# Kernel optimization log

Measured on AMD Instinct MI355X. Metric: run time of the kernel, lower is better.

## Reference

```python
import jax, jax.numpy as jnp
import numpy as np

N1 = 10000; N2 = 10000; F_IN = 256
E_EDGES = 480000; P_PAIRS = 200000
HID = 128; H = 8; DH = 16; L = 2


def _segment_softmax(logits, seg, n):
    # softmax over edges sharing the same destination node (per head)
    m = jax.ops.segment_max(logits, seg, num_segments=n)
    m = jnp.where(jnp.isfinite(m), m, 0.0)
    e = jnp.exp(logits - m[seg])
    s = jax.ops.segment_sum(e, seg, num_segments=n)
    return e / (s[seg] + 1e-16)


def _attend(q_dst, k_src, v_src, src, dst, arel, mrel, prior, n_dst):
    # q_dst: [Nd,H,D]; k_src/v_src: [Ns,H,D]; arel/mrel: [H,D,D]; prior: [H]
    k = jnp.einsum('nhd,hde->nhe', k_src, arel)[src]   # [E,H,D]
    v = jnp.einsum('nhd,hde->nhe', v_src, mrel)[src]   # [E,H,D]
    logits = jnp.einsum('ehd,ehd->eh', q_dst[dst], k) * prior / jnp.sqrt(jnp.asarray(DH, q_dst.dtype))
    a = _segment_softmax(logits, dst, n_dst)           # [E,H]
    out = jax.ops.segment_sum(a[..., None] * v, dst, num_segments=n_dst)
    return out.reshape(n_dst, HID)


def _forward(x_n1, x_n2, Win1, bin1, Win2, bin2, Wk, bk, Wq, bq, Wv, bv, Wa, ba, skip, arel, mrel, prior, ei12, ei21, edge_index):
    proj = lambda x, W, b: (x @ W + b).reshape(-1, H, DH)
    h1 = jax.nn.relu(x_n1 @ Win1 + bin1)
    h2 = jax.nn.relu(x_n2 @ Win2 + bin2)
    feats1, feats2 = [], []
    for l in range(L):
        k1, q1, v1 = proj(h1, Wk[l, 0], bk[l, 0]), proj(h1, Wq[l, 0], bq[l, 0]), proj(h1, Wv[l, 0], bv[l, 0])
        k2, q2, v2 = proj(h2, Wk[l, 1], bk[l, 1]), proj(h2, Wq[l, 1], bq[l, 1]), proj(h2, Wv[l, 1], bv[l, 1])
        # edge type 0: n1 -> n2 (dst = n2); edge type 1: n2 -> n1 (dst = n1)
        agg2 = _attend(q2, k1, v1, ei12[0], ei12[1], arel[l, 0], mrel[l, 0], prior[l, 0], N2)
        agg1 = _attend(q1, k2, v2, ei21[0], ei21[1], arel[l, 1], mrel[l, 1], prior[l, 1], N1)
        o1 = jax.nn.gelu(agg1) @ Wa[l, 0] + ba[l, 0]
        o2 = jax.nn.gelu(agg2) @ Wa[l, 1] + ba[l, 1]
        s1 = jax.nn.sigmoid(skip[l, 0]); s2 = jax.nn.sigmoid(skip[l, 1])
        h1 = s1 * o1 + (1.0 - s1) * h1
        h2 = s2 * o2 + (1.0 - s2) * h2
        feats1.append(h1); feats2.append(h2)
    Em = jnp.concatenate(feats1, axis=1)   # [N1, HID*L]
    Ed = jnp.concatenate(feats2, axis=1)   # [N2, HID*L]
    # scores = Em @ Ed.T then gather at (m_index, d_index); computed as gathered dot
    # products (same math, avoids [N1,N2] materialization). Dropout in eval mode.
    preds = jnp.einsum('pc,pc->p', Em[edge_index[0]], Ed[edge_index[1]])[:, None]
    return preds


def setup_inputs():
    key = jax.random.key(0)
    ks = jax.random.split(key, 16)
    sc = 0.05
    inp = {}
    inp['x_n1'] = jax.random.normal(ks[0], (N1, F_IN), jnp.float32)
    inp['x_n2'] = jax.random.normal(ks[1], (N2, F_IN), jnp.float32)
    inp['ei12'] = jnp.stack([jax.random.randint(ks[2], (E_EDGES,), 0, N1),
                             jax.random.randint(ks[3], (E_EDGES,), 0, N2)])
    inp['ei21'] = jnp.stack([jax.random.randint(ks[4], (E_EDGES,), 0, N2),
                             jax.random.randint(ks[5], (E_EDGES,), 0, N1)])
    inp['edge_index'] = jnp.stack([jax.random.randint(ks[6], (P_PAIRS,), 0, N1),
                                   jax.random.randint(ks[7], (P_PAIRS,), 0, N2)])
    inp['Win1'] = jax.random.normal(ks[8], (F_IN, HID), jnp.float32) * sc
    inp['bin1'] = jnp.zeros((HID,), jnp.float32)
    inp['Win2'] = jax.random.normal(ks[9], (F_IN, HID), jnp.float32) * sc
    inp['bin2'] = jnp.zeros((HID,), jnp.float32)
    inp['Wk'] = jax.random.normal(ks[10], (L, 2, HID, HID), jnp.float32) * sc
    inp['bk'] = jnp.zeros((L, 2, HID), jnp.float32)
    inp['Wq'] = jax.random.normal(ks[11], (L, 2, HID, HID), jnp.float32) * sc
    inp['bq'] = jnp.zeros((L, 2, HID), jnp.float32)
    inp['Wv'] = jax.random.normal(ks[12], (L, 2, HID, HID), jnp.float32) * sc
    inp['bv'] = jnp.zeros((L, 2, HID), jnp.float32)
    inp['Wa'] = jax.random.normal(ks[13], (L, 2, HID, HID), jnp.float32) * sc
    inp['ba'] = jnp.zeros((L, 2, HID), jnp.float32)
    inp['skip'] = jnp.ones((L, 2), jnp.float32)
    inp['arel'] = jax.random.normal(ks[14], (L, 2, H, DH, DH), jnp.float32) * 0.25
    inp['mrel'] = jax.random.normal(ks[15], (L, 2, H, DH, DH), jnp.float32) * 0.25
    inp['prior'] = jnp.ones((L, 2, H), jnp.float32)
    return inp


def reference(x_n1, x_n2, ei12, ei21, edge_index, Win1, bin1, Win2, bin2, Wk, bk, Wq, bq, Wv, bv, Wa, ba, skip, arel, mrel, prior):
    return _forward(x_n1, x_n2, Win1, bin1, Win2, bin2, Wk, bk, Wq, bq, Wv, bv, Wa, ba, skip, arel, mrel, prior, ei12, ei21, edge_index)
```

## Files before the change

### kernel.cpp

```cpp
#include <hip/hip_runtime.h>
#include <math.h>

#define N1c 10000
#define N2c 10000
#define F_INc 256
#define Ec 480000
#define Pc 200000
#define Lc 2
#define NPART 32
#define NPc 313
#define NBLK 256
#define CAPE 17408
#define CAPP 7936

using short8 = __attribute__((ext_vector_type(8))) short;
using float4v = __attribute__((ext_vector_type(4))) float;
using floatx2 = __attribute__((ext_vector_type(2))) float;

__device__ __forceinline__ float gelu_f(float x) {
    const float k0 = 0.7978845608028654f;
    const float k1 = 0.044715f;
    float x3 = x * x * x;
    float t = tanhf(k0 * (x + k1 * x3));
    return 0.5f * x * (1.0f + t);
}

__device__ __forceinline__ float bf2f(unsigned short x) {
    union { unsigned int u; float f; } c;
    c.u = ((unsigned int)x) << 16;
    return c.f;
}
__device__ __forceinline__ unsigned short f2bf(float f) {
    union { float f; unsigned int u; } c;
    c.f = f;
    unsigned int u = c.u;
    unsigned int r = (u + 0x7FFFu + ((u >> 16) & 1u)) >> 16;
    return (unsigned short)r;
}
__device__ __forceinline__ unsigned char f2fp8(float v) {
    unsigned int p = __builtin_amdgcn_cvt_pk_fp8_f32(v, v, 0u, false);
    return (unsigned char)(p & 0xFF);
}

__global__ __launch_bounds__(256) void prep_kernel(
    const float* __restrict__ Wq, const float* __restrict__ bq,
    const float* __restrict__ Wk, const float* __restrict__ bk,
    const float* __restrict__ Wv, const float* __restrict__ bv,
    const float* __restrict__ arel, const float* __restrict__ mrel,
    const float* __restrict__ prior,
    const float* __restrict__ Win1, const float* __restrict__ Win2,
    const float* __restrict__ Wa,
    short* __restrict__ Wqkvt, float* __restrict__ bqkv,
    short* __restrict__ Wint1, short* __restrict__ Wint2, short* __restrict__ Wat,
    int* __restrict__ gcnt)
{
    if (blockIdx.x == 0 && threadIdx.x < 3 * NPART) gcnt[threadIdx.x] = 0;
    int id = blockIdx.x * 256 + threadIdx.x;
    if (id < 196608) {
        int lt = id / 49152;
        int r = id - lt * 49152;
        int col = r >> 7, c = r & 127;
        short* Wout = Wqkvt + (size_t)lt * 384 * 128;
        float* bout = bqkv + lt * 384;
        if (col < 128) {
            Wout[col * 128 + c] = (short)f2bf(Wq[lt * 16384 + c * 128 + col]);
            if (c == 0) bout[col] = bq[lt * 128 + col];
            return;
        }
        int which = (col < 256) ? 0 : 1;
        int he = col - (which ? 256 : 128);
        int h = he >> 4, e = he & 15;
        const float* W = (which == 0 ? Wk : Wv) + lt * 16384;
        const float* b = (which == 0 ? bk : bv) + lt * 128;
        const float* R = (which == 0 ? arel : mrel) + lt * 2048;
        float sc = (which == 0) ? prior[lt * 8 + h] * 0.25f : 1.0f;
        float acc = 0.f;
        #pragma unroll
        for (int d = 0; d < 16; d++)
            acc += W[c * 128 + h * 16 + d] * R[(h * 16 + d) * 16 + e];
        Wout[col * 128 + c] = (short)f2bf(acc * sc);
        if (c == 0) {
            float bacc = 0.f;
            #pragma unroll
            for (int d = 0; d < 16; d++)
                bacc += b[h * 16 + d] * R[(h * 16 + d) * 16 + e];
            bout[col] = bacc * sc;
        }
    } else {
        int wid = id - 196608;
        if (wid < 65536) {
            int y = wid >> 15;
            int id2 = wid & 32767;
            int n = id2 >> 8, k = id2 & 255;
            const float* W = y ? Win2 : Win1;
            short* O = y ? Wint2 : Wint1;
            O[n * 256 + k] = (short)f2bf(W[k * 128 + n]);
        } else {
            int wid2 = wid - 65536;
            int lt = wid2 >> 14;
            int id2 = wid2 & 16383;
            int n = id2 >> 7, k = id2 & 127;
            Wat[lt * 16384 + n * 128 + k] = (short)f2bf(Wa[lt * 16384 + k * 128 + n]);
        }
    }
}

__global__ __launch_bounds__(256) void scatter_bins_kernel(
    const int* __restrict__ ei12, const int* __restrict__ ei21, const int* __restrict__ eidx,
    int* __restrict__ gcnt,
    unsigned int* __restrict__ stg12, unsigned int* __restrict__ stg21,
    unsigned int* __restrict__ stgm)
{
    int blk = blockIdx.x, z = blockIdx.y, t = threadIdx.x;
    const int* key; const int* pay; int E; unsigned int* stg; int cap;
    if (z == 0)      { key = ei12 + Ec; pay = ei12; E = Ec; stg = stg12; cap = CAPE; }
    else if (z == 1) { key = ei21 + Ec; pay = ei21; E = Ec; stg = stg21; cap = CAPE; }
    else             { key = eidx;      pay = nullptr; E = Pc; stg = stgm; cap = CAPP; }
    int chunk = (E + NBLK - 1) / NBLK;
    int start = blk * chunk;
    int stop = min(start + chunk, E);
    __shared__ int cnt[NPART];
    __shared__ int base[NPART];
    __shared__ int fill[NPART];
    if (t < NPART) cnt[t] = 0;
    __syncthreads();
    for (int e = start + t; e < stop; e += 256)
        atomicAdd(&cnt[key[e] / NPc], 1);
    __syncthreads();
    if (t < NPART) {
        base[t] = cnt[t] ? atomicAdd(&gcnt[z * NPART + t], cnt[t]) : 0;
        fill[t] = 0;
    }
    __syncthreads();
    for (int e = start + t; e < stop; e += 256) {
        unsigned int k = (unsigned int)key[e];
        int p = (int)(k / NPc);
        int r = atomicAdd(&fill[p], 1);
        unsigned int pk = (z == 2) ? ((k << 18) | (unsigned int)e)
                                   : ((k << 14) | (unsigned int)pay[e]);
        stg[(size_t)p * cap + base[p] + r] = pk;
    }
}

__global__ __launch_bounds__(256) void build_csr_kernel(
    const int* __restrict__ gcnt,
    const unsigned int* __restrict__ stg12, const unsigned int* __restrict__ stg21,
    const unsigned int* __restrict__ stgm,
    int* __restrict__ rp12, int* __restrict__ rp21, int* __restrict__ rpm,
    int* __restrict__ es12, int* __restrict__ es21, int* __restrict__ ps)
{
    int p = blockIdx.x, z = blockIdx.y, t = threadIdx.x;
    const unsigned int* stg; int* rowptr; int* out; int cap;
    if (z == 0)      { stg = stg12; rowptr = rp12; out = es12; cap = CAPE; }
    else if (z == 1) { stg = stg21; rowptr = rp21; out = es21; cap = CAPE; }
    else             { stg = stgm;  rowptr = rpm;  out = ps;   cap = CAPP; }
    int ksh = (z == 2) ? 18 : 14;
    unsigned int pmask = (z == 2) ? 0x3FFFFu : 0x3FFFu;
    int baseOut = 0, cntP = 0;
    #pragma unroll
    for (int j = 0; j < NPART; j++) {
        int c = gcnt[z * NPART + j];
        if (j < p) baseOut += c;
        if (j == p) cntP = c;
    }
    const unsigned int* sbase = stg + (size_t)p * cap;
    int lo = p * NPc;
    int hi = min(lo + NPc, 10000);

    __shared__ int hist[512];
    __shared__ int fill[NPc];
    hist[t] = 0; hist[t + 256] = 0;
    __syncthreads();
    for (int i = t; i < cntP; i += 256)
        atomicAdd(&hist[(int)(sbase[i] >> ksh) - lo], 1);
    __syncthreads();
    for (int off = 1; off < 512; off <<= 1) {
        int i0 = t, i1 = t + 256;
        int v0 = (i0 >= off) ? hist[i0 - off] : 0;
        int v1 = (i1 >= off) ? hist[i1 - off] : 0;
        __syncthreads();
        hist[i0] += v0; hist[i1] += v1;
        __syncthreads();
    }
    for (int i = t; i < NPc; i += 256) {
        int excl = i ? hist[i - 1] : 0;
        fill[i] = excl;
        if (lo + i < hi) rowptr[lo + i] = baseOut + excl;
    }
    if (p == NPART - 1 && t == 0) rowptr[10000] = baseOut + cntP;
    __syncthreads();
    for (int i = t; i < cntP; i += 256) {
        unsigned int pk = sbase[i];
        int r = atomicAdd(&fill[(int)(pk >> ksh) - lo], 1);
        out[baseOut + r] = (int)(pk & pmask);
    }
}

template<int A_GELU, int OUT_RELU, int SKIP, int PACKQKV, int ABF, int KT>
__global__ __launch_bounds__(256) void gemm_mfma(
    const void* __restrict__ A0v, const void* __restrict__ A1v, int ldA,
    const short* __restrict__ Wt0, const short* __restrict__ Wt1,
    const float* __restrict__ b0, const float* __restrict__ b1,
    unsigned short* __restrict__ C0, unsigned short* __restrict__ C1, int ldC,
    unsigned char* __restrict__ KV8o0, unsigned char* __restrict__ KV8o1,
    int M,
    const float* __restrict__ sk0, const float* __restrict__ sk1,
    const unsigned short* __restrict__ H0, const unsigned short* __restrict__ H1, int ldH)
{
    int z = blockIdx.z;
    const void* Av = z ? A1v : A0v;
    const short* Wt = z ? Wt1 : Wt0;
    const float* bias = z ? b1 : b0;
    unsigned short* C = z ? C1 : C0;
    unsigned char* KV8o = z ? KV8o1 : KV8o0;
    const float* skipv = z ? sk1 : sk0;
    const unsigned short* Hold = z ? H1 : H0;

    __shared__ short Alds[64 * 40];
    __shared__ short Blds[64 * 40];

    int tid = threadIdx.x;
    int w = tid >> 6;
    int l = tid & 63;
    int mBase = blockIdx.x * 64;
    int nBase = blockIdx.y * 64;

    int srow = tid >> 2;
    int koct = tid & 3;

    float4v acc[4];
    #pragma unroll
    for (int i = 0; i < 4; i++) acc[i] = (float4v){0.f, 0.f, 0.f, 0.f};

    int arow = mBase + srow;
    const short* Wptr = Wt + (size_t)(nBase + srow) * KT + koct * 8;

    int fl = l & 15;
    int fo = (l >> 4) * 8;

    #pragma unroll
    for (int k0 = 0; k0 < KT; k0 += 32) {
        uint4 raw;
        if (ABF) {
            const unsigned short* Ab = (const unsigned short*)Av;
            raw = make_uint4(0u, 0u, 0u, 0u);
            if (arow < M) raw = *(const uint4*)(Ab + (size_t)arow * ldA + k0 + koct * 8);
            if (A_GELU) {
                unsigned int wd[4] = {raw.x, raw.y, raw.z, raw.w};
                #pragma unroll
                for (int i = 0; i < 4; i++) {
                    float lo = gelu_f(bf2f((unsigned short)(wd[i] & 0xFFFFu)));
                    float hi = gelu_f(bf2f((unsigned short)(wd[i] >> 16)));
                    wd[i] = (unsigned int)f2bf(lo) | ((unsigned int)f2bf(hi) << 16);
                }
                raw = make_uint4(wd[0], wd[1], wd[2], wd[3]);
            }
        } else {
            const float* Af = (const float*)Av;
            float av[8];
            if (arow < M) {
                const float4* p = (const float4*)(Af + (size_t)arow * ldA + k0 + koct * 8);
                float4 f0 = p[0], f1 = p[1];
                av[0]=f0.x; av[1]=f0.y; av[2]=f0.z; av[3]=f0.w;
                av[4]=f1.x; av[5]=f1.y; av[6]=f1.z; av[7]=f1.w;
            } else {
                #pragma unroll
                for (int i = 0; i < 8; i++) av[i] = 0.f;
            }
            unsigned int pk[4];
            #pragma unroll
            for (int i = 0; i < 4; i++)
                pk[i] = (unsigned int)f2bf(av[2*i]) | ((unsigned int)f2bf(av[2*i+1]) << 16);
            raw = make_uint4(pk[0], pk[1], pk[2], pk[3]);
        }
        *(uint4*)&Alds[srow * 40 + koct * 8] = raw;
        *(uint4*)&Blds[srow * 40 + koct * 8] = *(const uint4*)(Wptr + k0);
        __syncthreads();

        short8 bfr = *(const short8*)&Blds[(w * 16 + fl) * 40 + fo];
        #pragma unroll
        for (int msub = 0; msub < 4; msub++) {
            short8 afr = *(const short8*)&Alds[(msub * 16 + fl) * 40 + fo];
            acc[msub] = __builtin_amdgcn_mfma_f32_16x16x32_bf16(afr, bfr, acc[msub], 0, 0, 0);
        }
        __syncthreads();
    }

    float sig = 0.f;
    if (SKIP) sig = 1.f / (1.f + __expf(-skipv[0]));
    int col = nBase + w * 16 + fl;
    float bcol = bias[col];
    int rbase = mBase + ((l >> 4) * 4);
    #pragma unroll
    for (int msub = 0; msub < 4; msub++) {
        #pragma unroll
        for (int r = 0; r < 4; r++) {
            int row = rbase + msub * 16 + r;
            if (row >= M) continue;
            float v = acc[msub][r] + bcol;
            if (OUT_RELU) v = fmaxf(v, 0.f);
            if (SKIP) v = sig * v + (1.f - sig) * bf2f(Hold[(size_t)row * ldH + col]);
            if (PACKQKV) {
                if (col < 128) {
                    C[(size_t)row * ldC + col] = f2bf(v);
                } else if (col < 256) {
                    int c = col - 128;
                    KV8o[(size_t)row * 256 + (c >> 3) * 16 + (c & 7)] = f2fp8(v);
                } else {
                    int c = col - 256;
                    KV8o[(size_t)row * 256 + (c >> 3) * 16 + 8 + (c & 7)] = f2fp8(v);
                }
            } else {
                C[(size_t)row * ldC + col] = f2bf(v);
            }
        }
    }
}

__global__ __launch_bounds__(128) void attend_kernel(
    const unsigned short* __restrict__ Qb1, const unsigned char* __restrict__ KV81,
    const unsigned short* __restrict__ Qb2, const unsigned char* __restrict__ KV82,
    const int* __restrict__ rp12, const int* __restrict__ es12,
    const int* __restrict__ rp21, const int* __restrict__ es21,
    unsigned short* __restrict__ agg1, unsigned short* __restrict__ agg2)
{
    int b = blockIdx.x;
    const unsigned short* Qb; const unsigned char* KV; const int* rp; const int* es;
    unsigned short* outb; int n;
    if (b < 1250) { n = b * 8 + (threadIdx.x >> 4);          Qb = Qb2; KV = KV81; rp = rp12; es = es12; outb = agg2; }
    else          { n = (b - 1250) * 8 + (threadIdx.x >> 4); Qb = Qb1; KV = KV82; rp = rp21; es = es21; outb = agg1; }
    int ln = threadIdx.x & 15;

    float q[8];
    {
        const ushort4* qp = (const ushort4*)(Qb + (size_t)n * 128 + 8 * ln);
        ushort4 qa = qp[0], qc = qp[1];
        q[0]=bf2f(qa.x); q[1]=bf2f(qa.y); q[2]=bf2f(qa.z); q[3]=bf2f(qa.w);
        q[4]=bf2f(qc.x); q[5]=bf2f(qc.y); q[6]=bf2f(qc.z); q[7]=bf2f(qc.w);
    }
    int beg = rp[n], end = rp[n + 1];
    float s = 0.f;
    float acc[8];
    #pragma unroll
    for (int c = 0; c < 8; c++) acc[c] = 0.f;

    auto dec8 = [&](unsigned int w0, unsigned int w1, float* d) {
        floatx2 a0 = __builtin_amdgcn_cvt_pk_f32_fp8(w0, false);
        floatx2 a1 = __builtin_amdgcn_cvt_pk_f32_fp8(w0, true);
        floatx2 a2 = __builtin_amdgcn_cvt_pk_f32_fp8(w1, false);
        floatx2 a3 = __builtin_amdgcn_cvt_pk_f32_fp8(w1, true);
        d[0]=a0[0]; d[1]=a0[1]; d[2]=a1[0]; d[3]=a1[1];
        d[4]=a2[0]; d[5]=a2[1]; d[6]=a3[0]; d[7]=a3[1];
    };
    auto proc1 = [&](uint4 kv) {
        float kd[8], vd[8];
        dec8(kv.x, kv.y, kd);
        float p = q[0]*kd[0] + q[1]*kd[1] + q[2]*kd[2] + q[3]*kd[3]
                + q[4]*kd[4] + q[5]*kd[5] + q[6]*kd[6] + q[7]*kd[7];
        p += __shfl_xor(p, 1, 2);
        float x = __expf(p);
        s += x;
        dec8(kv.z, kv.w, vd);
        #pragma unroll
        for (int c = 0; c < 8; c++) acc[c] += x * vd[c];
    };
    auto ld = [&](int e) { return *(const uint4*)(KV + (size_t)e * 256 + 16 * ln); };

    int i = beg;
    int pre = min(end, (beg + 3) & ~3);
    for (; i < pre; i++) proc1(ld(es[i]));
    for (; i + 8 <= end; i += 8) {
        int4 ea = *(const int4*)&es[i];
        int4 eb = *(const int4*)&es[i + 4];
        uint4 w0 = ld(ea.x), w1 = ld(ea.y), w2 = ld(ea.z), w3 = ld(ea.w);
        uint4 w4 = ld(eb.x), w5 = ld(eb.y), w6 = ld(eb.z), w7 = ld(eb.w);
        proc1(w0); proc1(w1); proc1(w2); proc1(w3);
        proc1(w4); proc1(w5); proc1(w6); proc1(w7);
    }
    for (; i + 4 <= end; i += 4) {
        int4 ea = *(const int4*)&es[i];
        uint4 w0 = ld(ea.x), w1 = ld(ea.y), w2 = ld(ea.z), w3 = ld(ea.w);
        proc1(w0); proc1(w1); proc1(w2); proc1(w3);
    }
    for (; i < end; i++) proc1(ld(es[i]));

    float inv = 1.f / (s + 1e-16f);
    unsigned int w0 = (unsigned int)f2bf(acc[0]*inv) | ((unsigned int)f2bf(acc[1]*inv) << 16);
    unsigned int w1 = (unsigned int)f2bf(acc[2]*inv) | ((unsigned int)f2bf(acc[3]*inv) << 16);
    unsigned int w2 = (unsigned int)f2bf(acc[4]*inv) | ((unsigned int)f2bf(acc[5]*inv) << 16);
    unsigned int w3 = (unsigned int)f2bf(acc[6]*inv) | ((unsigned int)f2bf(acc[7]*inv) << 16);
    *(uint4*)(outb + (size_t)n * 128 + 8 * ln) = make_uint4(w0, w1, w2, w3);
}

__global__ __launch_bounds__(256) void pred_kernel(
    const unsigned short* __restrict__ Emb, const unsigned short* __restrict__ Edb,
    const int* __restrict__ eidx,
    const int* __restrict__ rpm, const int* __restrict__ porder,
    float* __restrict__ out)
{
    int m = blockIdx.x * 4 + (threadIdx.x >> 6);
    int l = threadIdx.x & 63;
    int g = l >> 4;
    int ln = l & 15;
    int beg = rpm[m], end = rpm[m + 1];
    if (beg == end) return;
    float a[16];
    {
        const uint4* ap = (const uint4*)(Emb + (size_t)m * 256 + 16 * ln);
        uint4 u0 = ap[0], u1 = ap[1];
        unsigned int wv[8] = {u0.x, u0.y, u0.z, u0.w, u1.x, u1.y, u1.z, u1.w};
        #pragma unroll
        for (int i = 0; i < 8; i++) {
            a[2*i]   = bf2f((unsigned short)(wv[i] & 0xFFFFu));
            a[2*i+1] = bf2f((unsigned short)(wv[i] >> 16));
        }
    }
    for (int i = beg + g; i < end; i += 4) {
        int p = porder[i];
        int d = eidx[Pc + p];
        const uint4* bp = (const uint4*)(Edb + (size_t)d * 256 + 16 * ln);
        uint4 u0 = bp[0], u1 = bp[1];
        unsigned int wv[8] = {u0.x, u0.y, u0.z, u0.w, u1.x, u1.y, u1.z, u1.w};
        float s = 0.f;
        #pragma unroll
        for (int j = 0; j < 8; j++)
            s += a[2*j] * bf2f((unsigned short)(wv[j] & 0xFFFFu))
               + a[2*j+1] * bf2f((unsigned short)(wv[j] >> 16));
        s += __shfl_xor(s, 1, 16);
        s += __shfl_xor(s, 2, 16);
        s += __shfl_xor(s, 4, 16);
        s += __shfl_xor(s, 8, 16);
        if (ln == 0) out[p] = s;
    }
}

extern "C" void kernel_launch(void* const* d_in, const int* in_sizes, int n_in,
                              void* d_out, int out_size, void* d_ws, size_t ws_size,
                              hipStream_t stream)
{
    const float* x1   = (const float*)d_in[0];
    const float* x2   = (const float*)d_in[1];
    const int*   ei12 = (const int*)d_in[2];
    const int*   ei21 = (const int*)d_in[3];
    const int*   eidx = (const int*)d_in[4];
    const float* Win1 = (const float*)d_in[5];
    const float* bin1 = (const float*)d_in[6];
    const float* Win2 = (const float*)d_in[7];
    const float* bin2 = (const float*)d_in[8];
    const float* Wk   = (const float*)d_in[9];
    const float* bk   = (const float*)d_in[10];
    const float* Wq   = (const float*)d_in[11];
    const float* bq   = (const float*)d_in[12];
    const float* Wv   = (const float*)d_in[13];
    const float* bv   = (const float*)d_in[14];
    const float* Wa   = (const float*)d_in[15];
    const float* ba   = (const float*)d_in[16];
    const float* skip = (const float*)d_in[17];
    const float* arel = (const float*)d_in[18];
    const float* mrel = (const float*)d_in[19];
    const float* prior= (const float*)d_in[20];

    char* ws = (char*)d_ws;
    size_t off = 0;
    auto allocB = [&](size_t bytes) { void* p = ws + off; off += (bytes + 15) & ~15ull; return p; };
    auto allocF = [&](size_t n) { return (float*)allocB(n * 4); };
    auto allocI = [&](size_t n) { return (int*)allocB(n * 4); };
    auto allocS = [&](size_t n) { return (short*)allocB(n * 2); };
    auto allocU = [&](size_t n) { return (unsigned short*)allocB(n * 2); };

    unsigned short* h1b  = allocU((size_t)N1c * 128);
    unsigned short* h2b  = allocU((size_t)N2c * 128);
    unsigned short* Qb1  = allocU((size_t)N1c * 128);
    unsigned short* Qb2  = allocU((size_t)N2c * 128);
    unsigned char*  KV81 = (unsigned char*)allocB((size_t)N1c * 256);
    unsigned char*  KV82 = (unsigned char*)allocB((size_t)N2c * 256);
    unsigned short* agg1 = allocU((size_t)N1c * 128);
    unsigned short* agg2 = allocU((size_t)N2c * 128);
    unsigned short* Emb  = allocU((size_t)N1c * 256);
    unsigned short* Edb  = allocU((size_t)N2c * 256);
    float* bqkv  = allocF(4 * 384);
    short* Wqkvt = allocS(4 * 384 * 128);
    short* Wint1 = allocS(128 * 256);
    short* Wint2 = allocS(128 * 256);
    short* Wat   = allocS(4 * 128 * 128);
    int* rp12  = allocI(N2c + 1);
    int* rp21  = allocI(N1c + 1);
    int* rpm   = allocI(N1c + 1);
    int* es12  = allocI(Ec);
    int* es21  = allocI(Ec);
    int* ps    = allocI(Pc);
    int* gcnt  = allocI(3 * NPART);
    unsigned int* stg12 = (unsigned int*)allocB((size_t)NPART * CAPE * 4);
    unsigned int* stg21 = (unsigned int*)allocB((size_t)NPART * CAPE * 4);
    unsigned int* stgm  = (unsigned int*)allocB((size_t)NPART * CAPP * 4);

    prep_kernel<<<1280, 256, 0, stream>>>(
        Wq, bq, Wk, bk, Wv, bv, arel, mrel, prior,
        Win1, Win2, Wa, Wqkvt, bqkv, Wint1, Wint2, Wat, gcnt);

    scatter_bins_kernel<<<dim3(NBLK, 3), 256, 0, stream>>>(
        ei12, ei21, eidx, gcnt, stg12, stg21, stgm);
    build_csr_kernel<<<dim3(NPART, 3), 256, 0, stream>>>(
        gcnt, stg12, stg21, stgm, rp12, rp21, rpm, es12, es21, ps);

    const int MB = (N1c + 63) / 64;
    gemm_mfma<0, 1, 0, 0, 0, 256><<<dim3(MB, 2, 2), 256, 0, stream>>>(
        x1, x2, F_INc, Wint1, Wint2, bin1, bin2, h1b, h2b, 128,
        nullptr, nullptr,
        N1c, nullptr, nullptr, nullptr, nullptr, 0);

    for (int l = 0; l < Lc; l++) {
        const unsigned short* A1 = (l == 0) ? h1b : Emb;  int ld1 = (l == 0) ? 128 : 256;
        const unsigned short* A2 = (l == 0) ? h2b : Edb;
        int lt0 = l * 2 + 0, lt1 = l * 2 + 1;
        gemm_mfma<0, 0, 0, 1, 1, 128><<<dim3(MB, 6, 2), 256, 0, stream>>>(
            A1, A2, ld1,
            Wqkvt + (size_t)lt0 * 49152, Wqkvt + (size_t)lt1 * 49152,
            bqkv + lt0 * 384, bqkv + lt1 * 384,
            Qb1, Qb2, 128,
            KV81, KV82,
            N1c, nullptr, nullptr, nullptr, nullptr, 0);
        attend_kernel<<<(N1c + N2c) / 8, 128, 0, stream>>>(
            Qb1, KV81, Qb2, KV82, rp12, es12, rp21, es21, agg1, agg2);
        gemm_mfma<1, 0, 1, 0, 1, 128><<<dim3(MB, 2, 2), 256, 0, stream>>>(
            agg1, agg2, 128,
            Wat + (size_t)lt0 * 16384, Wat + (size_t)lt1 * 16384,
            ba + lt0 * 128, ba + lt1 * 128,
            Emb + l * 128, Edb + l * 128, 256,
            nullptr, nullptr,
            N1c,
            skip + lt0, skip + lt1,
            A1, A2, ld1);
    }

    pred_kernel<<<N1c / 4, 256, 0, stream>>>(Emb, Edb, eidx, rpm, ps, (float*)d_out);
}
```

Before: 304.4 us.

## Split attention edges across two half-waves and widen QKV GEMM tiles

The attend kernel now assigns 32 lanes per destination node instead of 16, with each 16-lane group processing half of the node's edge list. The partial sums and softmax denominators are then combined with a cross-lane shuffle. This doubles the parallelism available for gather latency, at the cost of twice as many blocks and extra shuffle work. Separately, the QKV GEMM gets an NS template parameter so each block computes two 64-column N-tiles, reusing the A tile from LDS across both and halving the number of blocks that reload A.

```diff
diff --git a/kernel.cpp b/kernel.cpp
--- a/kernel.cpp
+++ b/kernel.cpp
@@ -196,7 +196,7 @@
     }
 }
 
-template<int A_GELU, int OUT_RELU, int SKIP, int PACKQKV, int ABF, int KT>
+template<int A_GELU, int OUT_RELU, int SKIP, int PACKQKV, int ABF, int KT, int NS>
 __global__ __launch_bounds__(256) void gemm_mfma(
     const void* __restrict__ A0v, const void* __restrict__ A1v, int ldA,
     const short* __restrict__ Wt0, const short* __restrict__ Wt1,
@@ -217,23 +217,24 @@
     const unsigned short* Hold = z ? H1 : H0;
 
     __shared__ short Alds[64 * 40];
-    __shared__ short Blds[64 * 40];
+    __shared__ short Blds[64 * NS * 40];
 
     int tid = threadIdx.x;
     int w = tid >> 6;
     int l = tid & 63;
     int mBase = blockIdx.x * 64;
-    int nBase = blockIdx.y * 64;
+    int nBase = blockIdx.y * 64 * NS;
 
     int srow = tid >> 2;
     int koct = tid & 3;
 
-    float4v acc[4];
+    float4v acc[NS][4];
     #pragma unroll
-    for (int i = 0; i < 4; i++) acc[i] = (float4v){0.f, 0.f, 0.f, 0.f};
+    for (int s = 0; s < NS; s++)
+        #pragma unroll
+        for (int i = 0; i < 4; i++) acc[s][i] = (float4v){0.f, 0.f, 0.f, 0.f};
 
     int arow = mBase + srow;
-    const short* Wptr = Wt + (size_t)(nBase + srow) * KT + koct * 8;
 
     int fl = l & 15;
     int fo = (l >> 4) * 8;
@@ -274,44 +275,55 @@
             raw = make_uint4(pk[0], pk[1], pk[2], pk[3]);
         }
         *(uint4*)&Alds[srow * 40 + koct * 8] = raw;
-        *(uint4*)&Blds[srow * 40 + koct * 8] = *(const uint4*)(Wptr + k0);
+        #pragma unroll
+        for (int r = 0; r < NS; r++) {
+            int nrow = nBase + r * 64 + srow;
+            *(uint4*)&Blds[(r * 64 + srow) * 40 + koct * 8] =
+                *(const uint4*)(Wt + (size_t)nrow * KT + k0 + koct * 8);
+        }
         __syncthreads();
 
-        short8 bfr = *(const short8*)&Blds[(w * 16 + fl) * 40 + fo];
-        #pragma unroll
-        for (int msub = 0; msub < 4; msub++) {
-            short8 afr = *(const short8*)&Alds[(msub * 16 + fl) * 40 + fo];
-            acc[msub] = __builtin_amdgcn_mfma_f32_16x16x32_bf16(afr, bfr, acc[msub], 0, 0, 0);
+        #pragma unroll
+        for (int s = 0; s < NS; s++) {
+            short8 bfr = *(const short8*)&Blds[(s * 64 + w * 16 + fl) * 40 + fo];
+            #pragma unroll
+            for (int msub = 0; msub < 4; msub++) {
+                short8 afr = *(const short8*)&Alds[(msub * 16 + fl) * 40 + fo];
+                acc[s][msub] = __builtin_amdgcn_mfma_f32_16x16x32_bf16(afr, bfr, acc[s][msub], 0, 0, 0);
+            }
         }
         __syncthreads();
     }
 
     float sig = 0.f;
     if (SKIP) sig = 1.f / (1.f + __expf(-skipv[0]));
-    int col = nBase + w * 16 + fl;
-    float bcol = bias[col];
     int rbase = mBase + ((l >> 4) * 4);
     #pragma unroll
-    for (int msub = 0; msub < 4; msub++) {
-        #pragma unroll
-        for (int r = 0; r < 4; r++) {
-            int row = rbase + msub * 16 + r;
-            if (row >= M) continue;
-            float v = acc[msub][r] + bcol;
-            if (OUT_RELU) v = fmaxf(v, 0.f);
-            if (SKIP) v = sig * v + (1.f - sig) * bf2f(Hold[(size_t)row * ldH + col]);
-            if (PACKQKV) {
-                if (col < 128) {
+    for (int s = 0; s < NS; s++) {
+        int col = nBase + s * 64 + w * 16 + fl;
+        float bcol = bias[col];
+        #pragma unroll
+        for (int msub = 0; msub < 4; msub++) {
+            #pragma unroll
+            for (int r = 0; r < 4; r++) {
+                int row = rbase + msub * 16 + r;
+                if (row >= M) continue;
+                float v = acc[s][msub][r] + bcol;
+                if (OUT_RELU) v = fmaxf(v, 0.f);
+                if (SKIP) v = sig * v + (1.f - sig) * bf2f(Hold[(size_t)row * ldH + col]);
+                if (PACKQKV) {
+                    if (col < 128) {
+                        C[(size_t)row * ldC + col] = f2bf(v);
+                    } else if (col < 256) {
+                        int c = col - 128;
+                        KV8o[(size_t)row * 256 + (c >> 3) * 16 + (c & 7)] = f2fp8(v);
+                    } else {
+                        int c = col - 256;
+                        KV8o[(size_t)row * 256 + (c >> 3) * 16 + 8 + (c & 7)] = f2fp8(v);
+                    }
+                } else {
                     C[(size_t)row * ldC + col] = f2bf(v);
-                } else if (col < 256) {
-                    int c = col - 128;
-                    KV8o[(size_t)row * 256 + (c >> 3) * 16 + (c & 7)] = f2fp8(v);
-                } else {
-                    int c = col - 256;
-                    KV8o[(size_t)row * 256 + (c >> 3) * 16 + 8 + (c & 7)] = f2fp8(v);
                 }
-            } else {
-                C[(size_t)row * ldC + col] = f2bf(v);
             }
         }
     }
@@ -325,11 +337,14 @@
     unsigned short* __restrict__ agg1, unsigned short* __restrict__ agg2)
 {
     int b = blockIdx.x;
+    int nid = threadIdx.x >> 5;
+    int l32 = threadIdx.x & 31;
+    int g = l32 >> 4;
+    int ln = l32 & 15;
     const unsigned short* Qb; const unsigned char* KV; const int* rp; const int* es;
     unsigned short* outb; int n;
-    if (b < 1250) { n = b * 8 + (threadIdx.x >> 4);          Qb = Qb2; KV = KV81; rp = rp12; es = es12; outb = agg2; }
-    else          { n = (b - 1250) * 8 + (threadIdx.x >> 4); Qb = Qb1; KV = KV82; rp = rp21; es = es21; outb = agg1; }
-    int ln = threadIdx.x & 15;
+    if (b < 2500) { n = b * 4 + nid;          Qb = Qb2; KV = KV81; rp = rp12; es = es12; outb = agg2; }
+    else          { n = (b - 2500) * 4 + nid; Qb = Qb1; KV = KV82; rp = rp21; es = es21; outb = agg1; }
 
     float q[8];
     {
@@ -339,6 +354,11 @@
         q[4]=bf2f(qc.x); q[5]=bf2f(qc.y); q[6]=bf2f(qc.z); q[7]=bf2f(qc.w);
     }
     int beg = rp[n], end = rp[n + 1];
+    int cnt = end - beg;
+    int half = (cnt + 1) >> 1;
+    int gbeg = beg + g * half;
+    int gend = g ? end : (beg + half);
+
     float s = 0.f;
     float acc[8];
     #pragma unroll
@@ -366,10 +386,10 @@
     };
     auto ld = [&](int e) { return *(const uint4*)(KV + (size_t)e * 256 + 16 * ln); };
 
-    int i = beg;
-    int pre = min(end, (beg + 3) & ~3);
+    int i = gbeg;
+    int pre = min(gend, (gbeg + 3) & ~3);
     for (; i < pre; i++) proc1(ld(es[i]));
-    for (; i + 8 <= end; i += 8) {
+    for (; i + 8 <= gend; i += 8) {
         int4 ea = *(const int4*)&es[i];
         int4 eb = *(const int4*)&es[i + 4];
         uint4 w0 = ld(ea.x), w1 = ld(ea.y), w2 = ld(ea.z), w3 = ld(ea.w);
@@ -377,19 +397,25 @@
         proc1(w0); proc1(w1); proc1(w2); proc1(w3);
         proc1(w4); proc1(w5); proc1(w6); proc1(w7);
     }
-    for (; i + 4 <= end; i += 4) {
+    for (; i + 4 <= gend; i += 4) {
         int4 ea = *(const int4*)&es[i];
         uint4 w0 = ld(ea.x), w1 = ld(ea.y), w2 = ld(ea.z), w3 = ld(ea.w);
         proc1(w0); proc1(w1); proc1(w2); proc1(w3);
     }
-    for (; i < end; i++) proc1(ld(es[i]));
-
-    float inv = 1.f / (s + 1e-16f);
-    unsigned int w0 = (unsigned int)f2bf(acc[0]*inv) | ((unsigned int)f2bf(acc[1]*inv) << 16);
-    unsigned int w1 = (unsigned int)f2bf(acc[2]*inv) | ((unsigned int)f2bf(acc[3]*inv) << 16);
-    unsigned int w2 = (unsigned int)f2bf(acc[4]*inv) | ((unsigned int)f2bf(acc[5]*inv) << 16);
-    unsigned int w3 = (unsigned int)f2bf(acc[6]*inv) | ((unsigned int)f2bf(acc[7]*inv) << 16);
-    *(uint4*)(outb + (size_t)n * 128 + 8 * ln) = make_uint4(w0, w1, w2, w3);
+    for (; i < gend; i++) proc1(ld(es[i]));
+
+    s += __shfl_xor(s, 16, 32);
+    #pragma unroll
+    for (int c = 0; c < 8; c++) acc[c] += __shfl_xor(acc[c], 16, 32);
+
+    if (g == 0) {
+        float inv = 1.f / (s + 1e-16f);
+        unsigned int w0 = (unsigned int)f2bf(acc[0]*inv) | ((unsigned int)f2bf(acc[1]*inv) << 16);
+        unsigned int w1 = (unsigned int)f2bf(acc[2]*inv) | ((unsigned int)f2bf(acc[3]*inv) << 16);
+        unsigned int w2 = (unsigned int)f2bf(acc[4]*inv) | ((unsigned int)f2bf(acc[5]*inv) << 16);
+        unsigned int w3 = (unsigned int)f2bf(acc[6]*inv) | ((unsigned int)f2bf(acc[7]*inv) << 16);
+        *(uint4*)(outb + (size_t)n * 128 + 8 * ln) = make_uint4(w0, w1, w2, w3);
+    }
 }
 
 __global__ __launch_bounds__(256) void pred_kernel(
@@ -504,7 +530,7 @@
         gcnt, stg12, stg21, stgm, rp12, rp21, rpm, es12, es21, ps);
 
     const int MB = (N1c + 63) / 64;
-    gemm_mfma<0, 1, 0, 0, 0, 256><<<dim3(MB, 2, 2), 256, 0, stream>>>(
+    gemm_mfma<0, 1, 0, 0, 0, 256, 1><<<dim3(MB, 2, 2), 256, 0, stream>>>(
         x1, x2, F_INc, Wint1, Wint2, bin1, bin2, h1b, h2b, 128,
         nullptr, nullptr,
         N1c, nullptr, nullptr, nullptr, nullptr, 0);
@@ -513,16 +539,16 @@
         const unsigned short* A1 = (l == 0) ? h1b : Emb;  int ld1 = (l == 0) ? 128 : 256;
         const unsigned short* A2 = (l == 0) ? h2b : Edb;
         int lt0 = l * 2 + 0, lt1 = l * 2 + 1;
-        gemm_mfma<0, 0, 0, 1, 1, 128><<<dim3(MB, 6, 2), 256, 0, stream>>>(
+        gemm_mfma<0, 0, 0, 1, 1, 128, 2><<<dim3(MB, 3, 2), 256, 0, stream>>>(
             A1, A2, ld1,
             Wqkvt + (size_t)lt0 * 49152, Wqkvt + (size_t)lt1 * 49152,
             bqkv + lt0 * 384, bqkv + lt1 * 384,
             Qb1, Qb2, 128,
             KV81, KV82,
             N1c, nullptr, nullptr, nullptr, nullptr, 0);
-        attend_kernel<<<(N1c + N2c) / 8, 128, 0, stream>>>(
+        attend_kernel<<<(N1c + N2c) / 4, 128, 0, stream>>>(
             Qb1, KV81, Qb2, KV82, rp12, es12, rp21, es21, agg1, agg2);
-        gemm_mfma<1, 0, 1, 0, 1, 128><<<dim3(MB, 2, 2), 256, 0, stream>>>(
+        gemm_mfma<1, 0, 1, 0, 1, 128, 1><<<dim3(MB, 2, 2), 256, 0, stream>>>(
             agg1, agg2, 128,
             Wat + (size_t)lt0 * 16384, Wat + (size_t)lt1 * 16384,
             ba + lt0 * 128, ba + lt1 * 128,
```

Result: slower. 311.7 us (+2.4%).

## Co-schedule CSR build kernels with independent GEMMs in merged launches

Applied to the files above, without the earlier changes.

Turns the edge scatter, CSR build and GEMM kernels into device functions that take block indices and shared-memory pointers as arguments. The scatter-bins pass now shares one launch with the input-projection GEMM, and the CSR build shares one with the first-layer QKV GEMM. The aim is to cut launch count and let the small, latency-bound graph-preprocessing blocks run alongside the GEMM blocks instead of serially. The layer loop is unrolled by hand, and the shared-memory GEMM tile buffers are reused by the binning code. This adds branchy mixed-role kernels whose register use is set by the larger path.

```diff
diff --git a/kernel.cpp b/kernel.cpp
--- a/kernel.cpp
+++ b/kernel.cpp
@@ -105,13 +105,14 @@
     }
 }
 
-__global__ __launch_bounds__(256) void scatter_bins_kernel(
+__device__ void dev_scatter_bins(
+    int blk, int z, int* smem,
     const int* __restrict__ ei12, const int* __restrict__ ei21, const int* __restrict__ eidx,
     int* __restrict__ gcnt,
     unsigned int* __restrict__ stg12, unsigned int* __restrict__ stg21,
     unsigned int* __restrict__ stgm)
 {
-    int blk = blockIdx.x, z = blockIdx.y, t = threadIdx.x;
+    int t = threadIdx.x;
     const int* key; const int* pay; int E; unsigned int* stg; int cap;
     if (z == 0)      { key = ei12 + Ec; pay = ei12; E = Ec; stg = stg12; cap = CAPE; }
     else if (z == 1) { key = ei21 + Ec; pay = ei21; E = Ec; stg = stg21; cap = CAPE; }
@@ -119,9 +120,9 @@
     int chunk = (E + NBLK - 1) / NBLK;
     int start = blk * chunk;
     int stop = min(start + chunk, E);
-    __shared__ int cnt[NPART];
-    __shared__ int base[NPART];
-    __shared__ int fill[NPART];
+    int* cnt = smem;
+    int* base = smem + NPART;
+    int* fill = smem + 2 * NPART;
     if (t < NPART) cnt[t] = 0;
     __syncthreads();
     for (int e = start + t; e < stop; e += 256)
@@ -142,14 +143,15 @@
     }
 }
 
-__global__ __launch_bounds__(256) void build_csr_kernel(
+__device__ void dev_build_csr(
+    int p, int z, int* hist, int* fill,
     const int* __restrict__ gcnt,
     const unsigned int* __restrict__ stg12, const unsigned int* __restrict__ stg21,
     const unsigned int* __restrict__ stgm,
     int* __restrict__ rp12, int* __restrict__ rp21, int* __restrict__ rpm,
     int* __restrict__ es12, int* __restrict__ es21, int* __restrict__ ps)
 {
-    int p = blockIdx.x, z = blockIdx.y, t = threadIdx.x;
+    int t = threadIdx.x;
     const unsigned int* stg; int* rowptr; int* out; int cap;
     if (z == 0)      { stg = stg12; rowptr = rp12; out = es12; cap = CAPE; }
     else if (z == 1) { stg = stg21; rowptr = rp21; out = es21; cap = CAPE; }
@@ -167,8 +169,6 @@
     int lo = p * NPc;
     int hi = min(lo + NPc, 10000);
 
-    __shared__ int hist[512];
-    __shared__ int fill[NPc];
     hist[t] = 0; hist[t + 256] = 0;
     __syncthreads();
     for (int i = t; i < cntP; i += 256)
@@ -197,7 +197,8 @@
 }
 
 template<int A_GELU, int OUT_RELU, int SKIP, int PACKQKV, int ABF, int KT>
-__global__ __launch_bounds__(256) void gemm_mfma(
+__device__ void dev_gemm(
+    int mb, int ny, int z, short* Alds, short* Blds,
     const void* __restrict__ A0v, const void* __restrict__ A1v, int ldA,
     const short* __restrict__ Wt0, const short* __restrict__ Wt1,
     const float* __restrict__ b0, const float* __restrict__ b1,
@@ -207,7 +208,6 @@
     const float* __restrict__ sk0, const float* __restrict__ sk1,
     const unsigned short* __restrict__ H0, const unsigned short* __restrict__ H1, int ldH)
 {
-    int z = blockIdx.z;
     const void* Av = z ? A1v : A0v;
     const short* Wt = z ? Wt1 : Wt0;
     const float* bias = z ? b1 : b0;
@@ -216,14 +216,11 @@
     const float* skipv = z ? sk1 : sk0;
     const unsigned short* Hold = z ? H1 : H0;
 
-    __shared__ short Alds[64 * 40];
-    __shared__ short Blds[64 * 40];
-
     int tid = threadIdx.x;
     int w = tid >> 6;
     int l = tid & 63;
-    int mBase = blockIdx.x * 64;
-    int nBase = blockIdx.y * 64;
+    int mBase = mb * 64;
+    int nBase = ny * 64;
 
     int srow = tid >> 2;
     int koct = tid & 3;
@@ -317,6 +314,84 @@
     }
 }
 
+template<int A_GELU, int OUT_RELU, int SKIP, int PACKQKV, int ABF, int KT>
+__global__ __launch_bounds__(256) void gemm_mfma(
+    const void* __restrict__ A0v, const void* __restrict__ A1v, int ldA,
+    const short* __restrict__ Wt0, const short* __restrict__ Wt1,
+    const float* __restrict__ b0, const float* __restrict__ b1,
+    unsigned short* __restrict__ C0, unsigned short* __restrict__ C1, int ldC,
+    unsigned char* __restrict__ KV8o0, unsigned char* __restrict__ KV8o1,
+    int M,
+    const float* __restrict__ sk0, const float* __restrict__ sk1,
+    const unsigned short* __restrict__ H0, const unsigned short* __restrict__ H1, int ldH)
+{
+    __shared__ short Alds[64 * 40];
+    __shared__ short Blds[64 * 40];
+    dev_gemm<A_GELU, OUT_RELU, SKIP, PACKQKV, ABF, KT>(
+        blockIdx.x, blockIdx.y, blockIdx.z, Alds, Blds,
+        A0v, A1v, ldA, Wt0, Wt1, b0, b1, C0, C1, ldC,
+        KV8o0, KV8o1, M, sk0, sk1, H0, H1, ldH);
+}
+
+__global__ __launch_bounds__(256) void combo2_kernel(
+    const int* __restrict__ ei12, const int* __restrict__ ei21, const int* __restrict__ eidx,
+    int* __restrict__ gcnt,
+    unsigned int* __restrict__ stg12, unsigned int* __restrict__ stg21,
+    unsigned int* __restrict__ stgm,
+    const float* __restrict__ x1, const float* __restrict__ x2,
+    const short* __restrict__ Wint1, const short* __restrict__ Wint2,
+    const float* __restrict__ bin1, const float* __restrict__ bin2,
+    unsigned short* __restrict__ h1b, unsigned short* __restrict__ h2b)
+{
+    __shared__ short Alds[64 * 40];
+    __shared__ short Blds[64 * 40];
+    int bx = blockIdx.x;
+    if (bx < 768) {
+        dev_scatter_bins(bx & 255, bx >> 8, (int*)Alds,
+                         ei12, ei21, eidx, gcnt, stg12, stg21, stgm);
+    } else {
+        int idx = bx - 768;
+        int mb = idx % 157;
+        int r = idx / 157;
+        dev_gemm<0, 1, 0, 0, 0, 256>(
+            mb, r & 1, r >> 1, Alds, Blds,
+            x1, x2, F_INc, Wint1, Wint2, bin1, bin2,
+            h1b, h2b, 128, nullptr, nullptr,
+            N1c, nullptr, nullptr, nullptr, nullptr, 0);
+    }
+}
+
+__global__ __launch_bounds__(256) void combo3_kernel(
+    const int* __restrict__ gcnt,
+    const unsigned int* __restrict__ stg12, const unsigned int* __restrict__ stg21,
+    const unsigned int* __restrict__ stgm,
+    int* __restrict__ rp12, int* __restrict__ rp21, int* __restrict__ rpm,
+    int* __restrict__ es12, int* __restrict__ es21, int* __restrict__ ps,
+    const unsigned short* __restrict__ h1b, const unsigned short* __restrict__ h2b,
+    const short* __restrict__ Wqkvt0, const short* __restrict__ Wqkvt1,
+    const float* __restrict__ bqkv0, const float* __restrict__ bqkv1,
+    unsigned short* __restrict__ Qb1, unsigned short* __restrict__ Qb2,
+    unsigned char* __restrict__ KV81, unsigned char* __restrict__ KV82)
+{
+    __shared__ short Alds[64 * 40];
+    __shared__ short Blds[64 * 40];
+    int bx = blockIdx.x;
+    if (bx < 96) {
+        dev_build_csr(bx & 31, bx >> 5, (int*)Alds, (int*)Blds,
+                      gcnt, stg12, stg21, stgm,
+                      rp12, rp21, rpm, es12, es21, ps);
+    } else {
+        int idx = bx - 96;
+        int mb = idx % 157;
+        int r = idx / 157;
+        dev_gemm<0, 0, 0, 1, 1, 128>(
+            mb, r % 6, r / 6, Alds, Blds,
+            h1b, h2b, 128, Wqkvt0, Wqkvt1, bqkv0, bqkv1,
+            Qb1, Qb2, 128, KV81, KV82,
+            N1c, nullptr, nullptr, nullptr, nullptr, 0);
+    }
+}
+
 __global__ __launch_bounds__(128) void attend_kernel(
     const unsigned short* __restrict__ Qb1, const unsigned char* __restrict__ KV81,
     const unsigned short* __restrict__ Qb2, const unsigned char* __restrict__ KV82,
@@ -498,40 +573,43 @@
         Wq, bq, Wk, bk, Wv, bv, arel, mrel, prior,
         Win1, Win2, Wa, Wqkvt, bqkv, Wint1, Wint2, Wat, gcnt);
 
-    scatter_bins_kernel<<<dim3(NBLK, 3), 256, 0, stream>>>(
-        ei12, ei21, eidx, gcnt, stg12, stg21, stgm);
-    build_csr_kernel<<<dim3(NPART, 3), 256, 0, stream>>>(
-        gcnt, stg12, stg21, stgm, rp12, rp21, rpm, es12, es21, ps);
-
-    const int MB = (N1c + 63) / 64;
-    gemm_mfma<0, 1, 0, 0, 0, 256><<<dim3(MB, 2, 2), 256, 0, stream>>>(
-        x1, x2, F_INc, Wint1, Wint2, bin1, bin2, h1b, h2b, 128,
+    combo2_kernel<<<768 + 628, 256, 0, stream>>>(
+        ei12, ei21, eidx, gcnt, stg12, stg21, stgm,
+        x1, x2, Wint1, Wint2, bin1, bin2, h1b, h2b);
+
+    combo3_kernel<<<96 + 1884, 256, 0, stream>>>(
+        gcnt, stg12, stg21, stgm, rp12, rp21, rpm, es12, es21, ps,
+        h1b, h2b,
+        Wqkvt + 0 * 49152, Wqkvt + 1 * 49152,
+        bqkv + 0 * 384, bqkv + 1 * 384,
+        Qb1, Qb2, KV81, KV82);
+
+    attend_kernel<<<(N1c + N2c) / 8, 128, 0, stream>>>(
+        Qb1, KV81, Qb2, KV82, rp12, es12, rp21, es21, agg1, agg2);
+
+    gemm_mfma<1, 0, 1, 0, 1, 128><<<dim3(157, 2, 2), 256, 0, stream>>>(
+        agg1, agg2, 128,
+        Wat + 0 * 16384, Wat + 1 * 16384, ba + 0 * 128, ba + 1 * 128,
+        Emb, Edb, 256,
         nullptr, nullptr,
+        N1c, skip + 0, skip + 1, h1b, h2b, 128);
+
+    gemm_mfma<0, 0, 0, 1, 1, 128><<<dim3(157, 6, 2), 256, 0, stream>>>(
+        Emb, Edb, 256,
+        Wqkvt + 2 * 49152, Wqkvt + 3 * 49152,
+        bqkv + 2 * 384, bqkv + 3 * 384,
+        Qb1, Qb2, 128, KV81, KV82,
         N1c, nullptr, nullptr, nullptr, nullptr, 0);
 
-    for (int l = 0; l < Lc; l++) {
-        const unsigned short* A1 = (l == 0) ? h1b : Emb;  int ld1 = (l == 0) ? 128 : 256;
-        const unsigned short* A2 = (l == 0) ? h2b : Edb;
-        int lt0 = l * 2 + 0, lt1 = l * 2 + 1;
-        gemm_mfma<0, 0, 0, 1, 1, 128><<<dim3(MB, 6, 2), 256, 0, stream>>>(
-            A1, A2, ld1,
-            Wqkvt + (size_t)lt0 * 49152, Wqkvt + (size_t)lt1 * 49152,
-            bqkv + lt0 * 384, bqkv + lt1 * 384,
-            Qb1, Qb2, 128,
-            KV81, KV82,
-            N1c, nullptr, nullptr, nullptr, nullptr, 0);
-        attend_kernel<<<(N1c + N2c) / 8, 128, 0, stream>>>(
-            Qb1, KV81, Qb2, KV82, rp12, es12, rp21, es21, agg1, agg2);
-        gemm_mfma<1, 0, 1, 0, 1, 128><<<dim3(MB, 2, 2), 256, 0, stream>>>(
-            agg1, agg2, 128,
-            Wat + (size_t)lt0 * 16384, Wat + (size_t)lt1 * 16384,
-            ba + lt0 * 128, ba + lt1 * 128,
-            Emb + l * 128, Edb + l * 128, 256,
-            nullptr, nullptr,
-            N1c,
-            skip + lt0, skip + lt1,
-            A1, A2, ld1);
-    }
+    attend_kernel<<<(N1c + N2c) / 8, 128, 0, stream>>>(
+        Qb1, KV81, Qb2, KV82, rp12, es12, rp21, es21, agg1, agg2);
+
+    gemm_mfma<1, 0, 1, 0, 1, 128><<<dim3(157, 2, 2), 256, 0, stream>>>(
+        agg1, agg2, 128,
+        Wat + 2 * 16384, Wat + 3 * 16384, ba + 2 * 128, ba + 3 * 128,
+        Emb + 128, Edb + 128, 256,
+        nullptr, nullptr,
+        N1c, skip + 2, skip + 3, Emb, Edb, 256);
 
     pred_kernel<<<N1c / 4, 256, 0, stream>>>(Emb, Edb, eidx, rpm, ps, (float*)d_out);
 }
```

Result: faster. 290.6 us (-4.6%).
